# Optimization experiments

Measured on AMD Instinct MI355X. Metric: run time of the kernel, lower is better.

Reference implementation:

```python
import jax, jax.numpy as jnp
import numpy as np

B, S, H = 1, 2048, 4096
NH = 32
HD = H // NH  # 128
HALF = HD // 2
BASE = 10000.0


def setup_inputs() -> dict:
    key = jax.random.key(0)
    k1, k2, k3 = jax.random.split(key, 3)
    hidden_states = jax.random.normal(k1, (B, S, H), dtype=jnp.float32)
    W_qkv = jax.random.normal(k2, (H, 3 * H), dtype=jnp.float32) * 0.02
    W_o = jax.random.normal(k3, (H, H), dtype=jnp.float32) * 0.02
    # causal additive mask [B,1,S,S]: 0 on/below diagonal, large negative above
    causal = jnp.triu(jnp.full((S, S), -1e9, dtype=jnp.float32), k=1)
    attention_mask = jnp.broadcast_to(causal[None, None], (B, 1, S, S))
    position_ids = jnp.broadcast_to(jnp.arange(S, dtype=jnp.int64)[None, :], (B, S))
    return {
        'hidden_states': hidden_states,
        'W_qkv': W_qkv,
        'W_o': W_o,
        'attention_mask': attention_mask,
        'position_ids': position_ids,
    }


def _rope(x, cos, sin):
    # x: [b,s,nh,hd]; cos/sin: [b,s,1,half]. Half-split rotation as in the Triton kernel.
    x1, x2 = x[..., :HALF], x[..., HALF:]
    return jnp.concatenate([x1 * cos - x2 * sin, x1 * sin + x2 * cos], axis=-1)


def reference(hidden_states, W_qkv, W_o, attention_mask, position_ids):
    b, s, h = hidden_states.shape
    # fused QKV projection (dequantized GPTQ matmul == dense matmul math)
    qkv = jnp.einsum('bsh,hk->bsk', hidden_states, W_qkv).reshape(b, s, 3, NH, HD)
    # RoPE angles: freq = exp(col * INV_BASE) * position_id, INV_BASE = -2 ln(base)/head_dim
    inv_base = -2.0 * np.log(BASE) / HD
    freqs = jnp.exp(jnp.arange(HALF, dtype=jnp.float32) * inv_base)  # [half]
    theta = position_ids.astype(jnp.float32)[:, :, None] * freqs      # [b,s,half]
    cos = jnp.cos(theta)[:, :, None, :]
    sin = jnp.sin(theta)[:, :, None, :]
    q = _rope(qkv[:, :, 0], cos, sin).transpose(0, 2, 1, 3)  # [b,nh,s,hd]
    k = _rope(qkv[:, :, 1], cos, sin).transpose(0, 2, 1, 3)
    v = qkv[:, :, 2].transpose(0, 2, 1, 3)
    scores = jnp.einsum('bhqd,bhkd->bhqk', q, k) / np.sqrt(HD).astype(np.float32)
    scores = scores + attention_mask
    scores = jnp.maximum(scores, jnp.finfo(scores.dtype).min)
    attn = jax.nn.softmax(scores.astype(jnp.float32), axis=-1).astype(q.dtype)
    out = jnp.einsum('bhqk,bhkd->bqhd', attn, v).reshape(b, s, h)
    return jnp.einsum('bsh,ho->bso', out, W_o)
```

## Files before the change

kernel.cpp:

```cpp
#include <hip/hip_runtime.h>

#define S_LEN 2048
#define HDIM 4096
#define NHEADS 32
#define HEAD_DIM 128
#define HALF_DIM 64
#define N_QKV 12288
#define QK_COLS 8192

typedef __attribute__((ext_vector_type(8))) short short8;
typedef __attribute__((ext_vector_type(4))) float f32x4;

typedef const __attribute__((address_space(1))) unsigned int gu32;
typedef __attribute__((address_space(3))) unsigned int lu32;

__device__ __forceinline__ void gload_lds16(const void* g, void* l) {
    __builtin_amdgcn_global_load_lds((gu32*)g, (lu32*)l, 16, 0, 0);
}

__device__ __forceinline__ unsigned short f2bf(float f) {
    unsigned int u = __float_as_uint(f);
    u += 0x7fff + ((u >> 16) & 1);
    return (unsigned short)(u >> 16);
}

__device__ __forceinline__ void xcd_map(int& bx, int& by) {
    int gx = gridDim.x;
    int lin = blockIdx.y * gx + blockIdx.x;
    int x = lin & 7, c = lin >> 3;
    int bxp = gx >> 3;
    bx = bxp * x + c % bxp;
    by = c / bxp;
}


__global__ __launch_bounds__(256) void cvt_hs_k(const float* __restrict__ in,
                                                unsigned short* __restrict__ out, int n4) {
    int i = blockIdx.x * 256 + threadIdx.x;
    if (i >= n4) return;
    float4 v = reinterpret_cast<const float4*>(in)[i];
    ushort4 o;
    o.x = f2bf(v.x); o.y = f2bf(v.y); o.z = f2bf(v.z); o.w = f2bf(v.w);
    reinterpret_cast<ushort4*>(out)[i] = o;
}

__device__ __forceinline__ int permute_col(int n) {
    if (n < QK_COLS) {
        int hd = n & 127;
        int base = n - hd;
        int e = hd & 63;
        int d2 = (e & 15) + 32 * (e >> 4) + ((hd >> 6) << 4);
        return base + d2;
    }
    return n;
}

template <bool PERM>
__global__ __launch_bounds__(256) void tconv_k(const float* __restrict__ in,
                                               unsigned short* __restrict__ out, int R, int C) {
    __shared__ float tile[64][65];
    int c0 = blockIdx.x * 64, r0 = blockIdx.y * 64;
    int tx = threadIdx.x & 63, ty = threadIdx.x >> 6;
#pragma unroll
    for (int i = 0; i < 16; ++i) {
        int r = ty + i * 4;
        tile[r][tx] = in[(size_t)(r0 + r) * C + c0 + tx];
    }
    __syncthreads();
#pragma unroll
    for (int i = 0; i < 16; ++i) {
        int c = ty + i * 4;
        int n = PERM ? permute_col(c0 + c) : (c0 + c);
        out[(size_t)n * R + r0 + tx] = f2bf(tile[tx][c]);
    }
}

__global__ __launch_bounds__(256) void rope_tab_k(const int* __restrict__ pos_raw,
                                                  float* __restrict__ ctab,
                                                  float* __restrict__ stab) {
    int i = blockIdx.x * 256 + threadIdx.x;
    int s = i >> 6, d = i & 63;
    bool is64 = (pos_raw[1] == 0 && pos_raw[2] == 1);
    int p = is64 ? pos_raw[2 * s] : pos_raw[s];
    const float INVB = -0.14391156831212787f;
    float freq = expf((float)d * INVB);
    float th = (float)p * freq;
    ctab[i] = cosf(th);
    stab[i] = sinf(th);
}


__device__ __forceinline__ void mainloop(const unsigned short* __restrict__ Ag,
                                         const unsigned short* __restrict__ Bg,
                                         int K, int m0, int n0,
                                         char* As, char* Bs,
                                         f32x4 (&acc)[4][4]) {
    const int tid = threadIdx.x;
    const int wid = tid >> 6, lane = tid & 63, l15 = lane & 15, l4 = lane >> 4;
    const int wm = wid >> 1, wn = wid & 1;
    const int NT = K >> 6;

    size_t abase[4], bbase[4];
    int off[4];
#pragma unroll
    for (int i = 0; i < 4; ++i) {
        int p = (i * 256 + tid) << 4;
        int q = p ^ (((p >> 7) & 7) << 4);
        abase[i] = (size_t)(m0 + (q >> 7)) * K + ((q & 127) >> 1);
        bbase[i] = (size_t)(n0 + (q >> 7)) * K + ((q & 127) >> 1);
        off[i] = p;
    }

    for (int t = 0; t < NT; ++t) {
        int k0 = t << 6;
#pragma unroll
        for (int i = 0; i < 4; ++i) gload_lds16(Ag + abase[i] + k0, As + off[i]);
#pragma unroll
        for (int i = 0; i < 4; ++i) gload_lds16(Bg + bbase[i] + k0, Bs + off[i]);
        asm volatile("s_waitcnt vmcnt(0)" ::: "memory");
        __builtin_amdgcn_s_barrier();

        short8 a[4][2], b[4][2];
#pragma unroll
        for (int am = 0; am < 4; ++am)
#pragma unroll
            for (int ks = 0; ks < 2; ++ks) {
                int lin = ((wm * 64 + am * 16 + l15) << 7) + ks * 64 + l4 * 16;
                a[am][ks] = *(const short8*)(As + (lin ^ (((lin >> 7) & 7) << 4)));
            }
#pragma unroll
        for (int bn = 0; bn < 4; ++bn)
#pragma unroll
            for (int ks = 0; ks < 2; ++ks) {
                int lin = ((wn * 64 + bn * 16 + l15) << 7) + ks * 64 + l4 * 16;
                b[bn][ks] = *(const short8*)(Bs + (lin ^ (((lin >> 7) & 7) << 4)));
            }
#pragma unroll
        for (int ks = 0; ks < 2; ++ks)
#pragma unroll
            for (int am = 0; am < 4; ++am)
#pragma unroll
                for (int bn = 0; bn < 4; ++bn)
                    acc[am][bn] = __builtin_amdgcn_mfma_f32_16x16x32_bf16(a[am][ks], b[bn][ks], acc[am][bn], 0, 0, 0);

        __builtin_amdgcn_s_barrier();
    }
}

__global__ __launch_bounds__(256, 3) void gemm1_k(const unsigned short* __restrict__ A,
                                                  const unsigned short* __restrict__ Bt,
                                                  const float* __restrict__ ctab,
                                                  const float* __restrict__ stab,
                                                  unsigned short* __restrict__ qb,
                                                  unsigned short* __restrict__ kb,
                                                  unsigned short* __restrict__ vt) {
    __shared__ __attribute__((aligned(16))) char As[16384];
    __shared__ __attribute__((aligned(16))) char Bs[16384];

    int bx, by;
    xcd_map(bx, by);
    int m0 = by * 128, n0 = bx * 128;

    f32x4 acc[4][4];
#pragma unroll
    for (int i = 0; i < 4; ++i)
#pragma unroll
        for (int j = 0; j < 4; ++j) acc[i][j] = (f32x4){0.f, 0.f, 0.f, 0.f};

    mainloop(A, Bt, HDIM, m0, n0, As, Bs, acc);

    int tid = threadIdx.x, wid = tid >> 6, lane = tid & 63, l15 = lane & 15, l4 = lane >> 4;
    int wm = wid >> 1, wn = wid & 1;
    int which = n0 >> 12;
    int head = (n0 & 4095) >> 7;
    if (which < 2) {
        unsigned short* dst = which ? kb : qb;
#pragma unroll
        for (int am = 0; am < 4; ++am)
#pragma unroll
            for (int j = 0; j < 4; ++j) {
                int s = m0 + wm * 64 + am * 16 + l4 * 4 + j;
#pragma unroll
                for (int p = 0; p < 2; ++p) {
                    float x1 = acc[am][2 * p][j], x2 = acc[am][2 * p + 1][j];
                    int e = l15 + 16 * (2 * wn + p);
                    float cs = ctab[s * 64 + e], sn = stab[s * 64 + e];
                    dst[((size_t)head * S_LEN + s) * HEAD_DIM + e] = f2bf(x1 * cs - x2 * sn);
                    dst[((size_t)head * S_LEN + s) * HEAD_DIM + e + 64] = f2bf(x1 * sn + x2 * cs);
                }
            }
    } else {
#pragma unroll
        for (int am = 0; am < 4; ++am)
#pragma unroll
            for (int j = 0; j < 4; ++j) {
                int s = m0 + wm * 64 + am * 16 + l4 * 4 + j;
#pragma unroll
                for (int bn = 0; bn < 4; ++bn) {
                    int d = wn * 64 + bn * 16 + l15;
                    vt[((size_t)head * HEAD_DIM + d) * S_LEN + s] = f2bf(acc[am][bn][j]);
                }
            }
    }
}

__global__ __launch_bounds__(256, 3) void gemm2_k(const unsigned short* __restrict__ A,
                                                  const unsigned short* __restrict__ Bt,
                                                  float* __restrict__ out) {
    __shared__ __attribute__((aligned(16))) char As[16384];
    __shared__ __attribute__((aligned(16))) char Bs[16384];

    int bx, by;
    xcd_map(bx, by);
    int m0 = by * 128, n0 = bx * 128;

    f32x4 acc[4][4];
#pragma unroll
    for (int i = 0; i < 4; ++i)
#pragma unroll
        for (int j = 0; j < 4; ++j) acc[i][j] = (f32x4){0.f, 0.f, 0.f, 0.f};

    mainloop(A, Bt, HDIM, m0, n0, As, Bs, acc);

    int tid = threadIdx.x, wid = tid >> 6, lane = tid & 63, l15 = lane & 15, l4 = lane >> 4;
    int wm = wid >> 1, wn = wid & 1;
#pragma unroll
    for (int am = 0; am < 4; ++am)
#pragma unroll
        for (int j = 0; j < 4; ++j) {
            int s = m0 + wm * 64 + am * 16 + l4 * 4 + j;
#pragma unroll
            for (int bn = 0; bn < 4; ++bn)
                out[(size_t)s * HDIM + n0 + wn * 64 + bn * 16 + l15] = acc[am][bn][j];
        }
}

__global__ __launch_bounds__(256) void flash_k(const unsigned short* __restrict__ Q,
                                               const unsigned short* __restrict__ Kb,
                                               const unsigned short* __restrict__ Vt,
                                               unsigned short* __restrict__ Ctx) {
    __shared__ __attribute__((aligned(16))) unsigned short Ks[32 * 128];
    __shared__ __attribute__((aligned(16))) unsigned short Vs[128 * 32];
    __shared__ __attribute__((aligned(16))) unsigned short Ps[4][32 * 32];
    int qbk = blockIdx.x, h = blockIdx.y;
    int tid = threadIdx.x, w = tid >> 6, lane = tid & 63, l15 = lane & 15, l4 = lane >> 4;
    int qrow0 = qbk * 128 + w * 32;

    short8 qf[2][4];
#pragma unroll
    for (int mt = 0; mt < 2; ++mt) {
        int s = qrow0 + mt * 16 + l15;
#pragma unroll
        for (int ks = 0; ks < 4; ++ks)
            qf[mt][ks] = *(const short8*)(Q + ((size_t)h * S_LEN + s) * HEAD_DIM + ks * 32 + l4 * 8);
    }

    float m_run[2][4], l_run[2][4];
    f32x4 o[2][8];
#pragma unroll
    for (int mt = 0; mt < 2; ++mt)
#pragma unroll
        for (int j = 0; j < 4; ++j) { m_run[mt][j] = -1e30f; l_run[mt][j] = 0.f; }
#pragma unroll
    for (int mt = 0; mt < 2; ++mt)
#pragma unroll
        for (int dt = 0; dt < 8; ++dt) o[mt][dt] = (f32x4){0.f, 0.f, 0.f, 0.f};

    const float scale = 0.08838834764831845f;
    int ntiles = (qbk + 1) * 4;

    for (int t = 0; t < ntiles; ++t) {
        __syncthreads();
#pragma unroll
        for (int it = 0; it < 2; ++it) {
            int idx = it * 256 + tid;
            int kr = idx >> 4, kc = (idx & 15) << 3;
            gload_lds16(Kb + ((size_t)h * S_LEN + t * 32 + kr) * HEAD_DIM + kc, Ks + idx * 8);
            int vr = idx >> 2, vc = (idx & 3) << 3;
            gload_lds16(Vt + ((size_t)h * HEAD_DIM + vr) * S_LEN + t * 32 + vc, Vs + idx * 8);
        }
        __syncthreads();

        f32x4 sc[2][2];
#pragma unroll
        for (int mt = 0; mt < 2; ++mt)
#pragma unroll
            for (int nt = 0; nt < 2; ++nt) sc[mt][nt] = (f32x4){0.f, 0.f, 0.f, 0.f};
#pragma unroll
        for (int ks = 0; ks < 4; ++ks) {
            short8 kfr[2];
#pragma unroll
            for (int nt = 0; nt < 2; ++nt)
                kfr[nt] = *(const short8*)(Ks + (nt * 16 + l15) * 128 + ks * 32 + l4 * 8);
#pragma unroll
            for (int mt = 0; mt < 2; ++mt)
#pragma unroll
                for (int nt = 0; nt < 2; ++nt)
                    sc[mt][nt] = __builtin_amdgcn_mfma_f32_16x16x32_bf16(qf[mt][ks], kfr[nt], sc[mt][nt], 0, 0, 0);
        }

#pragma unroll
        for (int mt = 0; mt < 2; ++mt)
#pragma unroll
            for (int j = 0; j < 4; ++j) {
                int srow = qrow0 + mt * 16 + l4 * 4 + j;
                float v0 = sc[mt][0][j] * scale;
                float v1 = sc[mt][1][j] * scale;
                int c0 = t * 32 + l15;
                if (c0 > srow) v0 = -1e30f;
                if (c0 + 16 > srow) v1 = -1e30f;
                float mx = fmaxf(v0, v1);
                mx = fmaxf(mx, __shfl_xor(mx, 1));
                mx = fmaxf(mx, __shfl_xor(mx, 2));
                mx = fmaxf(mx, __shfl_xor(mx, 4));
                mx = fmaxf(mx, __shfl_xor(mx, 8));
                float mold = m_run[mt][j];
                float mnew = fmaxf(mold, mx);
                float r = __expf(mold - mnew);
                float p0 = __expf(v0 - mnew);
                float p1 = __expf(v1 - mnew);
                float rs = p0 + p1;
                rs += __shfl_xor(rs, 1);
                rs += __shfl_xor(rs, 2);
                rs += __shfl_xor(rs, 4);
                rs += __shfl_xor(rs, 8);
                m_run[mt][j] = mnew;
                l_run[mt][j] = l_run[mt][j] * r + rs;
#pragma unroll
                for (int dt = 0; dt < 8; ++dt) o[mt][dt][j] *= r;
                int prow = mt * 16 + l4 * 4 + j;
                Ps[w][prow * 32 + l15] = f2bf(p0);
                Ps[w][prow * 32 + l15 + 16] = f2bf(p1);
            }
        __syncthreads();

        short8 pf[2];
#pragma unroll
        for (int mt = 0; mt < 2; ++mt)
            pf[mt] = *(const short8*)(&Ps[w][(mt * 16 + l15) * 32 + l4 * 8]);
#pragma unroll
        for (int dt = 0; dt < 8; ++dt) {
            short8 vf = *(const short8*)(Vs + (dt * 16 + l15) * 32 + l4 * 8);
#pragma unroll
            for (int mt = 0; mt < 2; ++mt)
                o[mt][dt] = __builtin_amdgcn_mfma_f32_16x16x32_bf16(pf[mt], vf, o[mt][dt], 0, 0, 0);
        }
    }

#pragma unroll
    for (int mt = 0; mt < 2; ++mt)
#pragma unroll
        for (int j = 0; j < 4; ++j) {
            float inv = 1.0f / l_run[mt][j];
            int s = qrow0 + mt * 16 + l4 * 4 + j;
#pragma unroll
            for (int dt = 0; dt < 8; ++dt)
                Ctx[(size_t)s * HDIM + h * HEAD_DIM + dt * 16 + l15] = f2bf(o[mt][dt][j] * inv);
        }
}


extern "C" void kernel_launch(void* const* d_in, const int* in_sizes, int n_in,
                              void* d_out, int out_size, void* d_ws, size_t ws_size,
                              hipStream_t stream) {
    const float* hs = (const float*)d_in[0];
    const float* wqkv = (const float*)d_in[1];
    const float* wo = (const float*)d_in[2];
    const int* pos = (const int*)d_in[4];
    float* out = (float*)d_out;
    char* ws = (char*)d_ws;
    const size_t MB = 1024 * 1024;

    unsigned short* hs_b = (unsigned short*)(ws);
    unsigned short* wq_t = (unsigned short*)(ws + 16 * MB);
    unsigned short* wo_t = (unsigned short*)(ws + 112 * MB);
    unsigned short* qbuf = (unsigned short*)(ws + 144 * MB);
    unsigned short* kbuf = (unsigned short*)(ws + 160 * MB);
    unsigned short* vtb  = (unsigned short*)(ws + 176 * MB);
    unsigned short* ctx  = (unsigned short*)(ws + 192 * MB);
    float* ctab = (float*)(ws + 208 * MB);
    float* stab = (float*)(ws + 209 * MB);

    cvt_hs_k<<<(S_LEN * HDIM / 4 + 255) / 256, 256, 0, stream>>>(hs, hs_b, S_LEN * HDIM / 4);
    tconv_k<true><<<dim3(N_QKV / 64, HDIM / 64), 256, 0, stream>>>(wqkv, wq_t, HDIM, N_QKV);
    tconv_k<false><<<dim3(HDIM / 64, HDIM / 64), 256, 0, stream>>>(wo, wo_t, HDIM, HDIM);
    rope_tab_k<<<(S_LEN * 64) / 256, 256, 0, stream>>>(pos, ctab, stab);
    gemm1_k<<<dim3(N_QKV / 128, S_LEN / 128), 256, 0, stream>>>(hs_b, wq_t, ctab, stab, qbuf, kbuf, vtb);
    flash_k<<<dim3(S_LEN / 128, NHEADS), 256, 0, stream>>>(qbuf, kbuf, vtb, ctx);
    gemm2_k<<<dim3(HDIM / 128, S_LEN / 128), 256, 0, stream>>>(ctx, wo_t, out);
}
```

Measured before the change: 585.5 us.

## Double-buffer flash attention K/V tiles with swizzled LDS and lazy rescaling

Rewrites the flash attention inner loop to use 64-key tiles that are double-buffered in LDS through async global_load_lds, so the next tile's loads overlap with the current tile's MFMA work. LDS layouts for K, V and P are XOR-swizzled to avoid bank conflicts. Online-softmax rescaling is skipped unless some row's max rises by more than 8, and row sums are computed with an MFMA against a ones vector instead of shuffles. Heavy causal blocks are launched first. This uses more LDS, which may lower occupancy, and the hand-written vmcnt waits must match the loads actually issued.

```diff
diff --git a/kernel.cpp b/kernel.cpp
--- a/kernel.cpp
+++ b/kernel.cpp
@@ -239,13 +239,17 @@
                                                const unsigned short* __restrict__ Kb,
                                                const unsigned short* __restrict__ Vt,
                                                unsigned short* __restrict__ Ctx) {
-    __shared__ __attribute__((aligned(16))) unsigned short Ks[32 * 128];
-    __shared__ __attribute__((aligned(16))) unsigned short Vs[128 * 32];
-    __shared__ __attribute__((aligned(16))) unsigned short Ps[4][32 * 32];
-    int qbk = blockIdx.x, h = blockIdx.y;
+    __shared__ __attribute__((aligned(16))) char Ks[2][16384];
+    __shared__ __attribute__((aligned(16))) char Vs[2][16384];
+    __shared__ __attribute__((aligned(16))) char Ps[4][4096];
+    int qbk = (int)gridDim.x - 1 - blockIdx.x;
+    int h = blockIdx.y;
     int tid = threadIdx.x, w = tid >> 6, lane = tid & 63, l15 = lane & 15, l4 = lane >> 4;
     int qrow0 = qbk * 128 + w * 32;
 
+    const unsigned short* Kg = Kb + (size_t)h * S_LEN * HEAD_DIM;
+    const unsigned short* Vg = Vt + (size_t)h * HEAD_DIM * S_LEN;
+
     short8 qf[2][4];
 #pragma unroll
     for (int mt = 0; mt < 2; ++mt) {
@@ -255,103 +259,166 @@
             qf[mt][ks] = *(const short8*)(Q + ((size_t)h * S_LEN + s) * HEAD_DIM + ks * 32 + l4 * 8);
     }
 
-    float m_run[2][4], l_run[2][4];
+    float m_run[2][4];
     f32x4 o[2][8];
-#pragma unroll
-    for (int mt = 0; mt < 2; ++mt)
-#pragma unroll
-        for (int j = 0; j < 4; ++j) { m_run[mt][j] = -1e30f; l_run[mt][j] = 0.f; }
-#pragma unroll
-    for (int mt = 0; mt < 2; ++mt)
+    f32x4 lsum[2];
+#pragma unroll
+    for (int mt = 0; mt < 2; ++mt) {
+#pragma unroll
+        for (int j = 0; j < 4; ++j) m_run[mt][j] = -1e30f;
+        lsum[mt] = (f32x4){0.f, 0.f, 0.f, 0.f};
 #pragma unroll
         for (int dt = 0; dt < 8; ++dt) o[mt][dt] = (f32x4){0.f, 0.f, 0.f, 0.f};
+    }
+
+    int lofs[4];
+    size_t kgofs[4], vgofs[4];
+#pragma unroll
+    for (int i = 0; i < 4; ++i) {
+        int p = (i * 256 + tid) << 4;
+        lofs[i] = p;
+        int qk = p ^ (((p >> 8) & 7) << 4);
+        kgofs[i] = (size_t)(qk >> 8) * HEAD_DIM + ((qk & 255) >> 1);
+        int qv = p ^ (((p >> 7) & 7) << 4);
+        vgofs[i] = (size_t)(qv >> 7) * S_LEN + ((qv & 127) >> 1);
+    }
+
+    auto stage = [&](int t) {
+        char* Kd = Ks[t & 1];
+        char* Vd = Vs[t & 1];
+        size_t kvoff = (size_t)t * 64;
+#pragma unroll
+        for (int i = 0; i < 4; ++i) gload_lds16(Kg + kvoff * HEAD_DIM + kgofs[i], Kd + lofs[i]);
+#pragma unroll
+        for (int i = 0; i < 4; ++i) gload_lds16(Vg + kvoff + vgofs[i], Vd + lofs[i]);
+    };
 
     const float scale = 0.08838834764831845f;
-    int ntiles = (qbk + 1) * 4;
-
-    for (int t = 0; t < ntiles; ++t) {
-        __syncthreads();
-#pragma unroll
-        for (int it = 0; it < 2; ++it) {
-            int idx = it * 256 + tid;
-            int kr = idx >> 4, kc = (idx & 15) << 3;
-            gload_lds16(Kb + ((size_t)h * S_LEN + t * 32 + kr) * HEAD_DIM + kc, Ks + idx * 8);
-            int vr = idx >> 2, vc = (idx & 3) << 3;
-            gload_lds16(Vt + ((size_t)h * HEAD_DIM + vr) * S_LEN + t * 32 + vc, Vs + idx * 8);
-        }
-        __syncthreads();
-
-        f32x4 sc[2][2];
+    const int NT = 2 * (qbk + 1);
+
+    short8 onesv;
+#pragma unroll
+    for (int e = 0; e < 8; ++e) onesv[e] = (short)0x3F80;
+
+    stage(0);
+
+    for (int t = 0; t < NT; ++t) {
+        int cur = t & 1;
+        if (t + 1 < NT) {
+            stage(t + 1);
+            asm volatile("s_waitcnt vmcnt(8)" ::: "memory");
+        } else {
+            asm volatile("s_waitcnt vmcnt(0)" ::: "memory");
+        }
+        __builtin_amdgcn_sched_barrier(0);
+        __builtin_amdgcn_s_barrier();
+        __builtin_amdgcn_sched_barrier(0);
+
+        f32x4 sc[2][4];
 #pragma unroll
         for (int mt = 0; mt < 2; ++mt)
 #pragma unroll
-            for (int nt = 0; nt < 2; ++nt) sc[mt][nt] = (f32x4){0.f, 0.f, 0.f, 0.f};
+            for (int nt = 0; nt < 4; ++nt) sc[mt][nt] = (f32x4){0.f, 0.f, 0.f, 0.f};
 #pragma unroll
         for (int ks = 0; ks < 4; ++ks) {
-            short8 kfr[2];
-#pragma unroll
-            for (int nt = 0; nt < 2; ++nt)
-                kfr[nt] = *(const short8*)(Ks + (nt * 16 + l15) * 128 + ks * 32 + l4 * 8);
+            short8 kfr[4];
+#pragma unroll
+            for (int nt = 0; nt < 4; ++nt) {
+                int lin = ((nt * 16 + l15) << 8) + ks * 64 + l4 * 16;
+                kfr[nt] = *(const short8*)(Ks[cur] + (lin ^ (((lin >> 8) & 7) << 4)));
+            }
 #pragma unroll
             for (int mt = 0; mt < 2; ++mt)
 #pragma unroll
-                for (int nt = 0; nt < 2; ++nt)
+                for (int nt = 0; nt < 4; ++nt)
                     sc[mt][nt] = __builtin_amdgcn_mfma_f32_16x16x32_bf16(qf[mt][ks], kfr[nt], sc[mt][nt], 0, 0, 0);
         }
 
+        float pmax[2][4];
+        bool need = false;
 #pragma unroll
         for (int mt = 0; mt < 2; ++mt)
 #pragma unroll
             for (int j = 0; j < 4; ++j) {
                 int srow = qrow0 + mt * 16 + l4 * 4 + j;
-                float v0 = sc[mt][0][j] * scale;
-                float v1 = sc[mt][1][j] * scale;
-                int c0 = t * 32 + l15;
-                if (c0 > srow) v0 = -1e30f;
-                if (c0 + 16 > srow) v1 = -1e30f;
-                float mx = fmaxf(v0, v1);
+                int c = t * 64 + l15;
+                float v0 = (c      <= srow) ? sc[mt][0][j] * scale : -1e30f;
+                float v1 = (c + 16 <= srow) ? sc[mt][1][j] * scale : -1e30f;
+                float v2 = (c + 32 <= srow) ? sc[mt][2][j] * scale : -1e30f;
+                float v3 = (c + 48 <= srow) ? sc[mt][3][j] * scale : -1e30f;
+                sc[mt][0][j] = v0; sc[mt][1][j] = v1; sc[mt][2][j] = v2; sc[mt][3][j] = v3;
+                float mx = fmaxf(fmaxf(v0, v1), fmaxf(v2, v3));
                 mx = fmaxf(mx, __shfl_xor(mx, 1));
                 mx = fmaxf(mx, __shfl_xor(mx, 2));
                 mx = fmaxf(mx, __shfl_xor(mx, 4));
                 mx = fmaxf(mx, __shfl_xor(mx, 8));
-                float mold = m_run[mt][j];
-                float mnew = fmaxf(mold, mx);
-                float r = __expf(mold - mnew);
-                float p0 = __expf(v0 - mnew);
-                float p1 = __expf(v1 - mnew);
-                float rs = p0 + p1;
-                rs += __shfl_xor(rs, 1);
-                rs += __shfl_xor(rs, 2);
-                rs += __shfl_xor(rs, 4);
-                rs += __shfl_xor(rs, 8);
-                m_run[mt][j] = mnew;
-                l_run[mt][j] = l_run[mt][j] * r + rs;
-#pragma unroll
-                for (int dt = 0; dt < 8; ++dt) o[mt][dt][j] *= r;
+                pmax[mt][j] = mx;
+                need = need || (mx > m_run[mt][j] + 8.0f);
+            }
+        if (__any(need ? 1 : 0)) {
+#pragma unroll
+            for (int mt = 0; mt < 2; ++mt)
+#pragma unroll
+                for (int j = 0; j < 4; ++j) {
+                    float mnew = fmaxf(m_run[mt][j], pmax[mt][j]);
+                    float r = __expf(m_run[mt][j] - mnew);
+                    m_run[mt][j] = mnew;
+                    lsum[mt][j] *= r;
+#pragma unroll
+                    for (int dt = 0; dt < 8; ++dt) o[mt][dt][j] *= r;
+                }
+        }
+
+#pragma unroll
+        for (int mt = 0; mt < 2; ++mt)
+#pragma unroll
+            for (int j = 0; j < 4; ++j) {
                 int prow = mt * 16 + l4 * 4 + j;
-                Ps[w][prow * 32 + l15] = f2bf(p0);
-                Ps[w][prow * 32 + l15 + 16] = f2bf(p1);
-            }
-        __syncthreads();
-
-        short8 pf[2];
+                int rb = prow << 7;
+                int sw = (prow & 7) << 4;
+#pragma unroll
+                for (int nt = 0; nt < 4; ++nt) {
+                    unsigned short pb = f2bf(__expf(sc[mt][nt][j] - m_run[mt][j]));
+                    *(unsigned short*)(Ps[w] + ((rb + (l15 + nt * 16) * 2) ^ sw)) = pb;
+                }
+            }
+        asm volatile("s_waitcnt lgkmcnt(0)" ::: "memory");
+        __builtin_amdgcn_sched_barrier(0);
+
+        short8 pf[2][2];
 #pragma unroll
         for (int mt = 0; mt < 2; ++mt)
-            pf[mt] = *(const short8*)(&Ps[w][(mt * 16 + l15) * 32 + l4 * 8]);
+#pragma unroll
+            for (int k2 = 0; k2 < 2; ++k2) {
+                int lin = ((mt * 16 + l15) << 7) + k2 * 64 + l4 * 16;
+                pf[mt][k2] = *(const short8*)(Ps[w] + (lin ^ (((lin >> 7) & 7) << 4)));
+            }
+#pragma unroll
+        for (int k2 = 0; k2 < 2; ++k2)
+#pragma unroll
+            for (int mt = 0; mt < 2; ++mt)
+                lsum[mt] = __builtin_amdgcn_mfma_f32_16x16x32_bf16(pf[mt][k2], onesv, lsum[mt], 0, 0, 0);
 #pragma unroll
         for (int dt = 0; dt < 8; ++dt) {
-            short8 vf = *(const short8*)(Vs + (dt * 16 + l15) * 32 + l4 * 8);
-#pragma unroll
-            for (int mt = 0; mt < 2; ++mt)
-                o[mt][dt] = __builtin_amdgcn_mfma_f32_16x16x32_bf16(pf[mt], vf, o[mt][dt], 0, 0, 0);
-        }
+#pragma unroll
+            for (int k2 = 0; k2 < 2; ++k2) {
+                int lin = ((dt * 16 + l15) << 7) + k2 * 64 + l4 * 16;
+                short8 vf = *(const short8*)(Vs[cur] + (lin ^ (((lin >> 7) & 7) << 4)));
+#pragma unroll
+                for (int mt = 0; mt < 2; ++mt)
+                    o[mt][dt] = __builtin_amdgcn_mfma_f32_16x16x32_bf16(pf[mt][k2], vf, o[mt][dt], 0, 0, 0);
+            }
+        }
+        __builtin_amdgcn_sched_barrier(0);
+        __builtin_amdgcn_s_barrier();
+        __builtin_amdgcn_sched_barrier(0);
     }
 
 #pragma unroll
     for (int mt = 0; mt < 2; ++mt)
 #pragma unroll
         for (int j = 0; j < 4; ++j) {
-            float inv = 1.0f / l_run[mt][j];
+            float inv = 1.0f / lsum[mt][j];
             int s = qrow0 + mt * 16 + l4 * 4 + j;
 #pragma unroll
             for (int dt = 0; dt < 8; ++dt)
```

Result: no change. 591.3 us (+1.0%).
